# Kernel tuning notes

Measured on AMD Instinct MI355X. Metric: run time of the kernel, lower is better.

The kernel has to match this reference:

```python
import jax, jax.numpy as jnp
import numpy as np

N_NODES = 50000
N_EDGES = 800000
N_GRAPHS = 512
IN_DIM = 128
HID = 64


def setup_inputs() -> dict:
    key = jax.random.key(0)
    ks = jax.random.split(key, 12)
    x = jax.random.normal(ks[0], (N_NODES, IN_DIM), dtype=jnp.float32)
    edge_index = jax.random.randint(ks[1], (2, N_EDGES), 0, N_NODES, dtype=jnp.int64)
    batch = jnp.sort(jax.random.randint(ks[2], (N_NODES,), 0, N_GRAPHS, dtype=jnp.int64))

    def lin(k, fan_in, fan_out):
        # torch Linear default init: U(-1/sqrt(fan_in), 1/sqrt(fan_in)); stored as [in, out]
        bound = 1.0 / np.sqrt(fan_in)
        return jax.random.uniform(k, (fan_in, fan_out), minval=-bound, maxval=bound, dtype=jnp.float32)

    W1_1 = lin(ks[3], IN_DIM, HID)
    W2_1 = lin(ks[4], IN_DIM, HID)
    W1_2 = lin(ks[5], HID, HID)
    W2_2 = lin(ks[6], HID, HID)
    W1_3 = lin(ks[7], HID, HID)
    W2_3 = lin(ks[8], HID, HID)
    cW1 = lin(ks[9], HID, HID)
    cb1 = jnp.zeros((HID,), dtype=jnp.float32)
    cW2 = lin(ks[10], HID, 1)
    cb2 = jnp.zeros((1,), dtype=jnp.float32)
    return {"x": x, "edge_index": edge_index, "batch": batch,
            "W1_1": W1_1, "W2_1": W2_1, "W1_2": W1_2, "W2_2": W2_2,
            "W1_3": W1_3, "W2_3": W2_3, "cW1": cW1, "cb1": cb1,
            "cW2": cW2, "cb2": cb2}


def _gnn_layer(x, src, dst, W1, W2):
    # f(v) = relu( x[v] @ W1 + sum_{u in N(v)} x[u] @ W2 )
    self_part = x @ W1                      # [N, out]
    msg = x[src] @ W2                       # gather + matmul: [E, out]
    neigh = jax.ops.segment_sum(msg, dst, num_segments=N_NODES)  # scatter-add
    return jax.nn.relu(self_part + neigh)


def reference(x, edge_index, batch, W1_1, W2_1, W1_2, W2_2, W1_3, W2_3, cW1, cb1, cW2, cb2):
    src, dst = edge_index[0], edge_index[1]  # PyG source_to_target flow
    h = _gnn_layer(x, src, dst, W1_1, W2_1)
    h = _gnn_layer(h, src, dst, W1_2, W2_2)
    h = _gnn_layer(h, src, dst, W1_3, W2_3)
    # global_mean_pool over graph segments
    sums = jax.ops.segment_sum(h, batch, num_segments=N_GRAPHS)      # [G, HID]
    counts = jax.ops.segment_sum(jnp.ones((h.shape[0],), h.dtype), batch, num_segments=N_GRAPHS)
    pooled = sums / jnp.maximum(counts, 1.0)[:, None]
    # classifier MLP
    hcls = jax.nn.relu(pooled @ cW1 + cb1)
    return hcls @ cW2 + cb2                  # [G, 1]
```

## Files before the change

### kernel.cpp

```cpp
#include <hip/hip_runtime.h>


#define CAP 64

typedef __attribute__((ext_vector_type(8))) short short8;
typedef __attribute__((ext_vector_type(4))) float floatx4;
typedef __attribute__((ext_vector_type(2))) float floatx2;

__device__ __forceinline__ unsigned short f2bf(float f) {
    union { float f; unsigned u; } v; v.f = f;
    unsigned r = v.u + 0x7FFF + ((v.u >> 16) & 1);
    return (unsigned short)(r >> 16);
}

__device__ __forceinline__ unsigned char f2fp8(float f) {
    int v = __builtin_amdgcn_cvt_pk_fp8_f32(f, 0.f, 0, false);
    return (unsigned char)(v & 0xff);
}

__device__ __forceinline__ void fp8x8fma(float* t, uint2 w, float s) {
    floatx2 p;
    p = __builtin_amdgcn_cvt_pk_f32_fp8(w.x, false);
    t[0] = fmaf(p[0], s, t[0]); t[1] = fmaf(p[1], s, t[1]);
    p = __builtin_amdgcn_cvt_pk_f32_fp8(w.x, true);
    t[2] = fmaf(p[0], s, t[2]); t[3] = fmaf(p[1], s, t[3]);
    p = __builtin_amdgcn_cvt_pk_f32_fp8(w.y, false);
    t[4] = fmaf(p[0], s, t[4]); t[5] = fmaf(p[1], s, t[5]);
    p = __builtin_amdgcn_cvt_pk_f32_fp8(w.y, true);
    t[6] = fmaf(p[0], s, t[6]); t[7] = fmaf(p[1], s, t[7]);
}

__device__ __forceinline__ void bf8unpack(uint4 w, float* s) {
    s[0] = __uint_as_float(w.x << 16);
    s[1] = __uint_as_float(w.x & 0xffff0000u);
    s[2] = __uint_as_float(w.y << 16);
    s[3] = __uint_as_float(w.y & 0xffff0000u);
    s[4] = __uint_as_float(w.z << 16);
    s[5] = __uint_as_float(w.z & 0xffff0000u);
    s[6] = __uint_as_float(w.w << 16);
    s[7] = __uint_as_float(w.w & 0xffff0000u);
}

__device__ __forceinline__ void gather_deep(
    const unsigned char* __restrict__ M, const int* __restrict__ cnt,
    const unsigned short* __restrict__ csr, int node, int cg, float* acc8, int N)
{
    const int nodeC = node < N ? node : 0;
    int c = node < N ? cnt[nodeC] : 0;
    if (c > CAP) c = CAP;
    const uint4* bv = (const uint4*)(csr + (size_t)nodeC * CAP);

    uint4 q0 = bv[0];
    uint4 q1 = bv[1];
    unsigned idx[16];
    idx[0]  = q0.x & 0xffff; idx[1]  = q0.x >> 16;
    idx[2]  = q0.y & 0xffff; idx[3]  = q0.y >> 16;
    idx[4]  = q0.z & 0xffff; idx[5]  = q0.z >> 16;
    idx[6]  = q0.w & 0xffff; idx[7]  = q0.w >> 16;
    idx[8]  = q1.x & 0xffff; idx[9]  = q1.x >> 16;
    idx[10] = q1.y & 0xffff; idx[11] = q1.y >> 16;
    idx[12] = q1.z & 0xffff; idx[13] = q1.z >> 16;
    idx[14] = q1.w & 0xffff; idx[15] = q1.w >> 16;
#pragma unroll
    for (int j = 0; j < 16; ++j)
        if (j >= c) idx[j] = 0;

    uint2 w[16];
#pragma unroll
    for (int j = 0; j < 16; ++j)
        w[j] = *(const uint2*)&M[(size_t)idx[j] * 64 + cg * 8];

    float a[8], b[8];
#pragma unroll
    for (int j = 0; j < 8; ++j) { a[j] = 0.f; b[j] = 0.f; }
#pragma unroll
    for (int j = 0; j < 16; ++j)
        fp8x8fma((j & 1) ? b : a, w[j], (j < c) ? 1.f : 0.f);

    for (int base = 16; base < c; base += 8) {
        uint4 q = bv[base >> 3];
        unsigned id2[8];
        id2[0] = q.x & 0xffff; id2[1] = q.x >> 16;
        id2[2] = q.y & 0xffff; id2[3] = q.y >> 16;
        id2[4] = q.z & 0xffff; id2[5] = q.z >> 16;
        id2[6] = q.w & 0xffff; id2[7] = q.w >> 16;
#pragma unroll
        for (int j = 0; j < 8; ++j)
            if (base + j >= c) id2[j] = 0;
        uint2 w2[8];
#pragma unroll
        for (int j = 0; j < 8; ++j)
            w2[j] = *(const uint2*)&M[(size_t)id2[j] * 64 + cg * 8];
#pragma unroll
        for (int j = 0; j < 8; ++j)
            fp8x8fma((j & 1) ? b : a, w2[j], (base + j < c) ? 1.f : 0.f);
    }
#pragma unroll
    for (int j = 0; j < 8; ++j) acc8[j] = a[j] + b[j];
}


__device__ __forceinline__ void mm1_body(
    const float* __restrict__ Xraw,
    const float* __restrict__ W1, const float* __restrict__ W2,
    unsigned short* __restrict__ S, unsigned char* __restrict__ M,
    int N, int blk)
{
    __shared__ __align__(16) unsigned short Xs[64][72];
    __shared__ __align__(16) unsigned short Ws[128][72];
    const int tid  = threadIdx.x;
    const int lane = tid & 63;
    const int wv   = tid >> 6;
    const int lrow = lane & 15;
    const int quad = lane >> 4;
    const int row0 = blk * 64;

    floatx4 acc[8];
#pragma unroll
    for (int i = 0; i < 8; ++i) acc[i] = (floatx4){0.f, 0.f, 0.f, 0.f};

    const int xr  = tid >> 2;
    const int xk  = (tid & 3) * 16;
    const int gxr = row0 + xr;

    for (int ko = 0; ko < 128; ko += 64) {
#pragma unroll
        for (int q = 0; q < 4; ++q) {
            float4 v = make_float4(0.f, 0.f, 0.f, 0.f);
            if (gxr < N) v = *(const float4*)&Xraw[(size_t)gxr * 128 + ko + xk + q * 4];
            ushort4 p;
            p.x = f2bf(v.x); p.y = f2bf(v.y); p.z = f2bf(v.z); p.w = f2bf(v.w);
            *(ushort4*)&Xs[xr][xk + q * 4] = p;
        }
#pragma unroll
        for (int i = 0; i < 2; ++i) {
            int s  = tid + i * 256;
            int k0 = (s & 15) * 4;
            int c0 = (s >> 4) * 4;
            float wr[4][4];
#pragma unroll
            for (int r = 0; r < 4; ++r) {
                int gk = ko + k0 + r;
                float4 t4 = (c0 < 64) ? *(const float4*)&W1[(size_t)gk * 64 + c0]
                                      : *(const float4*)&W2[(size_t)gk * 64 + (c0 - 64)];
                wr[r][0] = t4.x; wr[r][1] = t4.y; wr[r][2] = t4.z; wr[r][3] = t4.w;
            }
#pragma unroll
            for (int j = 0; j < 4; ++j) {
                ushort4 col;
                col.x = f2bf(wr[0][j]); col.y = f2bf(wr[1][j]);
                col.z = f2bf(wr[2][j]); col.w = f2bf(wr[3][j]);
                *(ushort4*)&Ws[c0 + j][k0] = col;
            }
        }
        __syncthreads();

#pragma unroll
        for (int kc = 0; kc < 2; ++kc) {
            int kofs = kc * 32 + quad * 8;
            short8 a = *(const short8*)&Xs[wv * 16 + lrow][kofs];
#pragma unroll
            for (int ct = 0; ct < 8; ++ct) {
                short8 b = *(const short8*)&Ws[ct * 16 + lrow][kofs];
                acc[ct] = __builtin_amdgcn_mfma_f32_16x16x32_bf16(a, b, acc[ct], 0, 0, 0);
            }
        }
        __syncthreads();
    }

    const int orow = row0 + wv * 16 + quad * 4;
#pragma unroll
    for (int ct = 0; ct < 8; ++ct) {
        int col = ct * 16 + lrow;
#pragma unroll
        for (int r = 0; r < 4; ++r) {
            int gr = orow + r;
            if (gr < N) {
                if (ct < 4) S[(size_t)gr * 64 + col] = f2bf(acc[ct][r]);
                else        M[(size_t)gr * 64 + (col - 64)] = f2fp8(acc[ct][r]);
            }
        }
    }
}

__device__ __forceinline__ void fill_body(
    const int* __restrict__ ei, int* __restrict__ cnt,
    unsigned short* __restrict__ csr, int E, int bid, int stride)
{
    int base = bid * 256 + threadIdx.x;
    int e[8], d[8], s[8], p[8];
    bool v[8];
#pragma unroll
    for (int j = 0; j < 8; ++j) {
        e[j] = base + j * stride;
        v[j] = e[j] < E;
        if (v[j]) {
            d[j] = ei[E + e[j]];
            s[j] = ei[e[j]];
        }
    }
#pragma unroll
    for (int j = 0; j < 8; ++j)
        if (v[j]) p[j] = atomicAdd(&cnt[d[j]], 1);
#pragma unroll
    for (int j = 0; j < 8; ++j)
        if (v[j] && p[j] < CAP) csr[(size_t)d[j] * CAP + p[j]] = (unsigned short)s[j];
}

__global__ __launch_bounds__(256) void mm1_fill_kernel(
    const float* __restrict__ Xraw,
    const float* __restrict__ W1, const float* __restrict__ W2,
    unsigned short* __restrict__ S, unsigned char* __restrict__ M, int N,
    const int* __restrict__ ei, int* __restrict__ cnt,
    unsigned short* __restrict__ csr, int E, int edgeBlocks)
{
    if ((int)blockIdx.x < edgeBlocks) {
        fill_body(ei, cnt, csr, E, blockIdx.x, edgeBlocks * 256);
    } else {
        mm1_body(Xraw, W1, W2, S, M, N, (int)blockIdx.x - edgeBlocks);
    }
}

__global__ __launch_bounds__(256) void mm_gather_kernel(
    const unsigned short* __restrict__ Sprev, const unsigned char* __restrict__ Mprev,
    const int* __restrict__ cnt, const unsigned short* __restrict__ csr,
    const float* __restrict__ W1, const float* __restrict__ W2,
    unsigned short* __restrict__ Sout, unsigned char* __restrict__ Mout, int N)
{
    __shared__ __align__(16) unsigned short Xs[64][72];
    __shared__ __align__(16) unsigned short Ws[128][72];
    const int tid  = threadIdx.x;
    const int lane = tid & 63;
    const int wv   = tid >> 6;
    const int lrow = lane & 15;
    const int quad = lane >> 4;
    const int row0 = blockIdx.x * 64;
    const int eg   = lane >> 3;
    const int cg   = lane & 7;

#pragma unroll
    for (int i = 0; i < 2; ++i) {
        int s  = tid + i * 256;
        int k0 = (s & 15) * 4;
        int c0 = (s >> 4) * 4;
        float wr[4][4];
#pragma unroll
        for (int r = 0; r < 4; ++r) {
            int gk = k0 + r;
            float4 t4 = (c0 < 64) ? *(const float4*)&W1[(size_t)gk * 64 + c0]
                                  : *(const float4*)&W2[(size_t)gk * 64 + (c0 - 64)];
            wr[r][0] = t4.x; wr[r][1] = t4.y; wr[r][2] = t4.z; wr[r][3] = t4.w;
        }
#pragma unroll
        for (int j = 0; j < 4; ++j) {
            ushort4 col;
            col.x = f2bf(wr[0][j]); col.y = f2bf(wr[1][j]);
            col.z = f2bf(wr[2][j]); col.w = f2bf(wr[3][j]);
            *(ushort4*)&Ws[c0 + j][k0] = col;
        }
    }

#pragma unroll
    for (int half = 0; half < 2; ++half) {
        int xrow = half * 32 + wv * 8 + eg;
        int node = row0 + xrow;
        float g8[8];
        gather_deep(Mprev, cnt, csr, node, cg, g8, N);
        float r8[8];
        if (node < N) {
            uint4 h = *(const uint4*)&Sprev[(size_t)node * 64 + cg * 8];
            float s8[8];
            bf8unpack(h, s8);
#pragma unroll
            for (int j = 0; j < 8; ++j) r8[j] = fmaxf(g8[j] + s8[j], 0.f);
        } else {
#pragma unroll
            for (int j = 0; j < 8; ++j) r8[j] = 0.f;
        }
        ushort4 p0, p1;
        p0.x = f2bf(r8[0]); p0.y = f2bf(r8[1]); p0.z = f2bf(r8[2]); p0.w = f2bf(r8[3]);
        p1.x = f2bf(r8[4]); p1.y = f2bf(r8[5]); p1.z = f2bf(r8[6]); p1.w = f2bf(r8[7]);
        *(ushort4*)&Xs[xrow][cg * 8]     = p0;
        *(ushort4*)&Xs[xrow][cg * 8 + 4] = p1;
    }
    __syncthreads();

    floatx4 acc[8];
#pragma unroll
    for (int i = 0; i < 8; ++i) acc[i] = (floatx4){0.f, 0.f, 0.f, 0.f};
#pragma unroll
    for (int kc = 0; kc < 2; ++kc) {
        int kofs = kc * 32 + quad * 8;
        short8 a = *(const short8*)&Xs[wv * 16 + lrow][kofs];
#pragma unroll
        for (int ct = 0; ct < 8; ++ct) {
            short8 b = *(const short8*)&Ws[ct * 16 + lrow][kofs];
            acc[ct] = __builtin_amdgcn_mfma_f32_16x16x32_bf16(a, b, acc[ct], 0, 0, 0);
        }
    }

    const int orow = row0 + wv * 16 + quad * 4;
#pragma unroll
    for (int ct = 0; ct < 8; ++ct) {
        int col = ct * 16 + lrow;
#pragma unroll
        for (int r = 0; r < 4; ++r) {
            int gr = orow + r;
            if (gr < N) {
                if (ct < 4) Sout[(size_t)gr * 64 + col] = f2bf(acc[ct][r]);
                else        Mout[(size_t)gr * 64 + (col - 64)] = f2fp8(acc[ct][r]);
            }
        }
    }
}

__global__ __launch_bounds__(512) void pool_gather_cls_kernel(
    const unsigned short* __restrict__ S, const unsigned char* __restrict__ M,
    const int* __restrict__ cnt, const unsigned short* __restrict__ csr,
    const int* __restrict__ batch,
    const float* __restrict__ cW1, const float* __restrict__ cb1,
    const float* __restrict__ cW2, const float* __restrict__ cb2,
    float* __restrict__ out, int N)
{
    int g  = blockIdx.x;
    int t  = threadIdx.x;
    int wv = t >> 6;
    int lane = t & 63;
    int eg = lane >> 3;
    int cg = lane & 7;
    int slot = wv * 8 + eg;

    int lo = 0, hi = N;
    while (lo < hi) { int mid = (lo + hi) >> 1; if (batch[mid] < g) lo = mid + 1; else hi = mid; }
    int start = lo;
    hi = N;
    while (lo < hi) { int mid = (lo + hi) >> 1; if (batch[mid] < g + 1) lo = mid + 1; else hi = mid; }
    int end = lo;

    float p8[8];
#pragma unroll
    for (int j = 0; j < 8; ++j) p8[j] = 0.f;

    for (int r = start + slot; r < end; r += 64) {
        float g8[8];
        gather_deep(M, cnt, csr, r, cg, g8, N);
        uint4 h = *(const uint4*)&S[(size_t)r * 64 + cg * 8];
        float s8[8];
        bf8unpack(h, s8);
#pragma unroll
        for (int j = 0; j < 8; ++j) p8[j] += fmaxf(g8[j] + s8[j], 0.f);
    }

    __shared__ float part[64][64];
    __shared__ float pooled[64];
#pragma unroll
    for (int j = 0; j < 8; ++j) part[slot][cg * 8 + j] = p8[j];
    __syncthreads();

    if (t < 64) {
        float s = 0.f;
#pragma unroll 8
        for (int k = 0; k < 64; ++k) s += part[k][t];
        float c_ = (float)((end - start) > 0 ? (end - start) : 1);
        pooled[t] = s / c_;
    }
    __syncthreads();
    if (t < 64) {
        float a = cb1[t];
#pragma unroll 8
        for (int k = 0; k < 64; ++k) a += pooled[k] * cW1[k * 64 + t];
        a = fmaxf(a, 0.f);
        float o = a * cW2[t];
#pragma unroll
        for (int off_ = 32; off_ > 0; off_ >>= 1) o += __shfl_down(o, off_);
        if (t == 0) out[g] = o + cb2[0];
    }
}

extern "C" void kernel_launch(void* const* d_in, const int* in_sizes, int n_in,
                              void* d_out, int out_size, void* d_ws, size_t ws_size,
                              hipStream_t stream)
{
    const float* x     = (const float*)d_in[0];
    const int*   ei    = (const int*)d_in[1];
    const int*   batch = (const int*)d_in[2];
    const float* W1_1  = (const float*)d_in[3];
    const float* W2_1  = (const float*)d_in[4];
    const float* W1_2  = (const float*)d_in[5];
    const float* W2_2  = (const float*)d_in[6];
    const float* W1_3  = (const float*)d_in[7];
    const float* W2_3  = (const float*)d_in[8];
    const float* cW1   = (const float*)d_in[9];
    const float* cb1   = (const float*)d_in[10];
    const float* cW2   = (const float*)d_in[11];
    const float* cb2   = (const float*)d_in[12];
    float* out = (float*)d_out;

    const int N = in_sizes[0] / 128;
    const int E = in_sizes[1] / 2;
    const int G = out_size;

    unsigned char*  MA  = (unsigned char*)d_ws;
    unsigned char*  MB  = MA + (size_t)N * 64;
    unsigned short* SA  = (unsigned short*)(MB + (size_t)N * 64);
    unsigned short* SB  = SA + (size_t)N * 64;
    int*            cnt = (int*)(SB + (size_t)N * 64);
    unsigned short* csr = (unsigned short*)(cnt + N);

    const int mmGrid     = (N + 63) / 64;
    const int edgeBlocks = (E + 2047) / 2048;

    hipMemsetAsync(cnt, 0, (size_t)N * sizeof(int), stream);

    mm1_fill_kernel<<<edgeBlocks + mmGrid, 256, 0, stream>>>(
        x, W1_1, W2_1, SA, MA, N, ei, cnt, csr, E, edgeBlocks);
    mm_gather_kernel<<<mmGrid, 256, 0, stream>>>(
        SA, MA, cnt, csr, W1_2, W2_2, SB, MB, N);
    mm_gather_kernel<<<mmGrid, 256, 0, stream>>>(
        SB, MB, cnt, csr, W1_3, W2_3, SA, MA, N);
    pool_gather_cls_kernel<<<G, 512, 0, stream>>>(
        SA, MA, cnt, csr, batch, cW1, cb1, cW2, cb2, out, N);
}
```

Before: 206.6 us.

## Embed per-node edge count in CSR row header and deepen unrolled gather

Moves the per-node neighbor count into the first 4 bytes of each node's 128-byte CSR row, so the gather reads count and indices in one contiguous load instead of a separate count array. The fixed unrolled gather now covers 30 neighbors instead of 16, since the average in-degree is about 16 and the tail loop runs less often. In exchange the memset now clears the whole CSR region, per-row capacity drops to 62, and more loads are issued for low-degree nodes.

```diff
diff --git a/kernel.cpp b/kernel.cpp
--- a/kernel.cpp
+++ b/kernel.cpp
@@ -1,7 +1,7 @@
 #include <hip/hip_runtime.h>
 
 
-#define CAP 64
+#define NSLOT 62
 
 typedef __attribute__((ext_vector_type(8))) short short8;
 typedef __attribute__((ext_vector_type(4))) float floatx4;
@@ -41,44 +41,59 @@
     s[7] = __uint_as_float(w.w & 0xffff0000u);
 }
 
-__device__ __forceinline__ void gather_deep(
-    const unsigned char* __restrict__ M, const int* __restrict__ cnt,
-    const unsigned short* __restrict__ csr, int node, int cg, float* acc8, int N)
+__device__ __forceinline__ void gather_row(
+    const unsigned char* __restrict__ M, const unsigned short* __restrict__ csrx,
+    int node, int cg, float* acc8, int N)
 {
     const int nodeC = node < N ? node : 0;
-    int c = node < N ? cnt[nodeC] : 0;
-    if (c > CAP) c = CAP;
-    const uint4* bv = (const uint4*)(csr + (size_t)nodeC * CAP);
-
-    uint4 q0 = bv[0];
-    uint4 q1 = bv[1];
-    unsigned idx[16];
-    idx[0]  = q0.x & 0xffff; idx[1]  = q0.x >> 16;
-    idx[2]  = q0.y & 0xffff; idx[3]  = q0.y >> 16;
-    idx[4]  = q0.z & 0xffff; idx[5]  = q0.z >> 16;
-    idx[6]  = q0.w & 0xffff; idx[7]  = q0.w >> 16;
-    idx[8]  = q1.x & 0xffff; idx[9]  = q1.x >> 16;
-    idx[10] = q1.y & 0xffff; idx[11] = q1.y >> 16;
-    idx[12] = q1.z & 0xffff; idx[13] = q1.z >> 16;
-    idx[14] = q1.w & 0xffff; idx[15] = q1.w >> 16;
+    const uint4* bv = (const uint4*)(csrx + (size_t)nodeC * 64);
+    uint4 q0 = bv[0], q1 = bv[1], q2 = bv[2], q3 = bv[3];
+    int c = node < N ? (int)q0.x : 0;
+    if (c > NSLOT) c = NSLOT;
+
+    unsigned ia[16], ib[14];
+    ia[0]  = q0.y & 0xffff; ia[1]  = q0.y >> 16;
+    ia[2]  = q0.z & 0xffff; ia[3]  = q0.z >> 16;
+    ia[4]  = q0.w & 0xffff; ia[5]  = q0.w >> 16;
+    ia[6]  = q1.x & 0xffff; ia[7]  = q1.x >> 16;
+    ia[8]  = q1.y & 0xffff; ia[9]  = q1.y >> 16;
+    ia[10] = q1.z & 0xffff; ia[11] = q1.z >> 16;
+    ia[12] = q1.w & 0xffff; ia[13] = q1.w >> 16;
+    ia[14] = q2.x & 0xffff; ia[15] = q2.x >> 16;
+    ib[0]  = q2.y & 0xffff; ib[1]  = q2.y >> 16;
+    ib[2]  = q2.z & 0xffff; ib[3]  = q2.z >> 16;
+    ib[4]  = q2.w & 0xffff; ib[5]  = q2.w >> 16;
+    ib[6]  = q3.x & 0xffff; ib[7]  = q3.x >> 16;
+    ib[8]  = q3.y & 0xffff; ib[9]  = q3.y >> 16;
+    ib[10] = q3.z & 0xffff; ib[11] = q3.z >> 16;
+    ib[12] = q3.w & 0xffff; ib[13] = q3.w >> 16;
+
+#pragma unroll
+    for (int j = 0; j < 16; ++j) if (j >= c) ia[j] = 0;
+#pragma unroll
+    for (int j = 0; j < 14; ++j) if (16 + j >= c) ib[j] = 0;
+
+    uint2 wa[16];
 #pragma unroll
     for (int j = 0; j < 16; ++j)
-        if (j >= c) idx[j] = 0;
-
-    uint2 w[16];
+        wa[j] = *(const uint2*)&M[(size_t)ia[j] * 64 + cg * 8];
+    uint2 wb[14];
+#pragma unroll
+    for (int j = 0; j < 14; ++j)
+        wb[j] = *(const uint2*)&M[(size_t)ib[j] * 64 + cg * 8];
+
+    float a[8], b[8];
+#pragma unroll
+    for (int j = 0; j < 8; ++j) { a[j] = 0.f; b[j] = 0.f; }
 #pragma unroll
     for (int j = 0; j < 16; ++j)
-        w[j] = *(const uint2*)&M[(size_t)idx[j] * 64 + cg * 8];
-
-    float a[8], b[8];
-#pragma unroll
-    for (int j = 0; j < 8; ++j) { a[j] = 0.f; b[j] = 0.f; }
-#pragma unroll
-    for (int j = 0; j < 16; ++j)
-        fp8x8fma((j & 1) ? b : a, w[j], (j < c) ? 1.f : 0.f);
-
-    for (int base = 16; base < c; base += 8) {
-        uint4 q = bv[base >> 3];
+        fp8x8fma((j & 1) ? b : a, wa[j], (j < c) ? 1.f : 0.f);
+#pragma unroll
+    for (int j = 0; j < 14; ++j)
+        fp8x8fma((j & 1) ? b : a, wb[j], (16 + j < c) ? 1.f : 0.f);
+
+    for (int base = 30; base < c; base += 8) {
+        uint4 q = bv[4 + ((base - 30) >> 3)];
         unsigned id2[8];
         id2[0] = q.x & 0xffff; id2[1] = q.x >> 16;
         id2[2] = q.y & 0xffff; id2[3] = q.y >> 16;
@@ -184,8 +199,8 @@
 }
 
 __device__ __forceinline__ void fill_body(
-    const int* __restrict__ ei, int* __restrict__ cnt,
-    unsigned short* __restrict__ csr, int E, int bid, int stride)
+    const int* __restrict__ ei, unsigned short* __restrict__ csrx,
+    int E, int bid, int stride)
 {
     int base = bid * 256 + threadIdx.x;
     int e[8], d[8], s[8], p[8];
@@ -201,21 +216,21 @@
     }
 #pragma unroll
     for (int j = 0; j < 8; ++j)
-        if (v[j]) p[j] = atomicAdd(&cnt[d[j]], 1);
+        if (v[j]) p[j] = atomicAdd((int*)(csrx + (size_t)d[j] * 64), 1);
 #pragma unroll
     for (int j = 0; j < 8; ++j)
-        if (v[j] && p[j] < CAP) csr[(size_t)d[j] * CAP + p[j]] = (unsigned short)s[j];
+        if (v[j] && p[j] < NSLOT) csrx[(size_t)d[j] * 64 + 2 + p[j]] = (unsigned short)s[j];
 }
 
 __global__ __launch_bounds__(256) void mm1_fill_kernel(
     const float* __restrict__ Xraw,
     const float* __restrict__ W1, const float* __restrict__ W2,
     unsigned short* __restrict__ S, unsigned char* __restrict__ M, int N,
-    const int* __restrict__ ei, int* __restrict__ cnt,
-    unsigned short* __restrict__ csr, int E, int edgeBlocks)
+    const int* __restrict__ ei, unsigned short* __restrict__ csrx,
+    int E, int edgeBlocks)
 {
     if ((int)blockIdx.x < edgeBlocks) {
-        fill_body(ei, cnt, csr, E, blockIdx.x, edgeBlocks * 256);
+        fill_body(ei, csrx, E, blockIdx.x, edgeBlocks * 256);
     } else {
         mm1_body(Xraw, W1, W2, S, M, N, (int)blockIdx.x - edgeBlocks);
     }
@@ -223,7 +238,7 @@
 
 __global__ __launch_bounds__(256) void mm_gather_kernel(
     const unsigned short* __restrict__ Sprev, const unsigned char* __restrict__ Mprev,
-    const int* __restrict__ cnt, const unsigned short* __restrict__ csr,
+    const unsigned short* __restrict__ csrx,
     const float* __restrict__ W1, const float* __restrict__ W2,
     unsigned short* __restrict__ Sout, unsigned char* __restrict__ Mout, int N)
 {
@@ -265,7 +280,7 @@
         int xrow = half * 32 + wv * 8 + eg;
         int node = row0 + xrow;
         float g8[8];
-        gather_deep(Mprev, cnt, csr, node, cg, g8, N);
+        gather_row(Mprev, csrx, node, cg, g8, N);
         float r8[8];
         if (node < N) {
             uint4 h = *(const uint4*)&Sprev[(size_t)node * 64 + cg * 8];
@@ -316,7 +331,7 @@
 
 __global__ __launch_bounds__(512) void pool_gather_cls_kernel(
     const unsigned short* __restrict__ S, const unsigned char* __restrict__ M,
-    const int* __restrict__ cnt, const unsigned short* __restrict__ csr,
+    const unsigned short* __restrict__ csrx,
     const int* __restrict__ batch,
     const float* __restrict__ cW1, const float* __restrict__ cb1,
     const float* __restrict__ cW2, const float* __restrict__ cb2,
@@ -343,7 +358,7 @@
 
     for (int r = start + slot; r < end; r += 64) {
         float g8[8];
-        gather_deep(M, cnt, csr, r, cg, g8, N);
+        gather_row(M, csrx, r, cg, g8, N);
         uint4 h = *(const uint4*)&S[(size_t)r * 64 + cg * 8];
         float s8[8];
         bf8unpack(h, s8);
@@ -400,24 +415,23 @@
     const int E = in_sizes[1] / 2;
     const int G = out_size;
 
-    unsigned char*  MA  = (unsigned char*)d_ws;
-    unsigned char*  MB  = MA + (size_t)N * 64;
-    unsigned short* SA  = (unsigned short*)(MB + (size_t)N * 64);
-    unsigned short* SB  = SA + (size_t)N * 64;
-    int*            cnt = (int*)(SB + (size_t)N * 64);
-    unsigned short* csr = (unsigned short*)(cnt + N);
+    unsigned char*  MA   = (unsigned char*)d_ws;
+    unsigned char*  MB   = MA + (size_t)N * 64;
+    unsigned short* SA   = (unsigned short*)(MB + (size_t)N * 64);
+    unsigned short* SB   = SA + (size_t)N * 64;
+    unsigned short* csrx = SB + (size_t)N * 64;
 
     const int mmGrid     = (N + 63) / 64;
     const int edgeBlocks = (E + 2047) / 2048;
 
-    hipMemsetAsync(cnt, 0, (size_t)N * sizeof(int), stream);
+    (void)hipMemsetAsync(csrx, 0, (size_t)N * 64 * sizeof(unsigned short), stream);
 
     mm1_fill_kernel<<<edgeBlocks + mmGrid, 256, 0, stream>>>(
-        x, W1_1, W2_1, SA, MA, N, ei, cnt, csr, E, edgeBlocks);
+        x, W1_1, W2_1, SA, MA, N, ei, csrx, E, edgeBlocks);
     mm_gather_kernel<<<mmGrid, 256, 0, stream>>>(
-        SA, MA, cnt, csr, W1_2, W2_2, SB, MB, N);
+        SA, MA, csrx, W1_2, W2_2, SB, MB, N);
     mm_gather_kernel<<<mmGrid, 256, 0, stream>>>(
-        SB, MB, cnt, csr, W1_3, W2_3, SA, MA, N);
+        SB, MB, csrx, W1_3, W2_3, SA, MA, N);
     pool_gather_cls_kernel<<<G, 512, 0, stream>>>(
-        SA, MA, cnt, csr, batch, cW1, cb1, cW2, cb2, out, N);
-}
+        SA, MA, csrx, batch, cW1, cb1, cW2, cb2, out, N);
+}
```

After: 200.5 us. -2.9%, faster.
